# Kernel optimization log

Hardware: AMD Instinct MI355X
Metric: run time of the kernel (lower is better)

The kernel has to match this reference:

```python
import jax, jax.numpy as jnp
import numpy as np
import math

H, NH, LAT = 2048, 16, 512
D = H // NH  # head_dim = 128
B, S = 2, 2048


def setup_inputs() -> dict:
    key = jax.random.key(0)
    ks = jax.random.split(key, 18)
    w = lambda k, i, o: jax.random.normal(k, (i, o), dtype=jnp.float32) * 0.02
    inp = {
        'hidden_states': jax.random.normal(ks[0], (B, S, H), dtype=jnp.float32),
        'attention_mask': jnp.ones((B, S), dtype=jnp.int32),
        'W_DKV': w(ks[1], H, LAT), 'b_DKV': jnp.zeros((LAT,), jnp.float32),
        'W_DQ': w(ks[2], H, LAT), 'b_DQ': jnp.zeros((LAT,), jnp.float32),
        'W_UK': w(ks[3], LAT, H), 'b_UK': jnp.zeros((H,), jnp.float32),
        'W_UV': w(ks[4], LAT, H), 'b_UV': jnp.zeros((H,), jnp.float32),
        'W_UQ': w(ks[5], LAT, H), 'b_UQ': jnp.zeros((H,), jnp.float32),
        'W_KR': w(ks[6], H, D), 'b_KR': jnp.zeros((D,), jnp.float32),
        'W_QR': w(ks[7], H, D), 'b_QR': jnp.zeros((D,), jnp.float32),
        'W_O': w(ks[8], H, H), 'b_O': jnp.zeros((H,), jnp.float32),
    }
    return inp


def _rope(x, seq_len):
    # x: [B, S, D]; rotate-half RoPE exactly as the torch module
    half = D // 2
    inv_freq = 1.0 / (10000.0 ** (jnp.arange(0, D, 2, dtype=jnp.float32) / D))
    ang = jnp.arange(seq_len, dtype=jnp.float32)[:, None] * inv_freq[None, :]  # [S, half]
    sin, cos = jnp.sin(ang), jnp.cos(ang)
    x1, x2 = x[..., :half], x[..., half:]
    return jnp.concatenate([x1 * cos - x2 * sin, x1 * sin + x2 * cos], axis=-1)


def reference(hidden_states, attention_mask, W_DKV, b_DKV, W_DQ, b_DQ,
              W_UK, b_UK, W_UV, b_UV, W_UQ, b_UQ,
              W_KR, b_KR, W_QR, b_QR, W_O, b_O):
    b, s, _ = hidden_states.shape
    c_kv = hidden_states @ W_DKV + b_DKV          # [B,S,LAT]
    c_q = hidden_states @ W_DQ + b_DQ
    k_c = (c_kv @ W_UK + b_UK).reshape(b, s, NH, D).transpose(0, 2, 1, 3)  # [B,H,S,D]
    v_c = (c_kv @ W_UV + b_UV).reshape(b, s, NH, D).transpose(0, 2, 1, 3)
    q_c = (c_q @ W_UQ + b_UQ).reshape(b, s, NH, D).transpose(0, 2, 1, 3)
    k_r = _rope(hidden_states @ W_KR + b_KR, s)[:, None]  # [B,1,S,D] shared across heads
    q_r = _rope(hidden_states @ W_QR + b_QR, s)[:, None]
    scale = 1.0 / math.sqrt(D)
    # q·k with concatenated [compressed | rope] head layout, decomposed to avoid materializing cat
    scores = (jnp.einsum('bhqd,bhkd->bhqk', q_c, k_c)
              + jnp.einsum('bhqd,bhkd->bhqk', q_r, k_r)) * scale  # [B,H,S,S]
    mask = attention_mask[:, None, None, :]
    scores = jnp.where(mask == 0, -jnp.inf, scores)
    attn = jax.nn.softmax(scores, axis=-1)
    ctx = jnp.einsum('bhqk,bhkd->bhqd', attn, v_c)
    ctx = ctx.transpose(0, 2, 1, 3).reshape(b, s, H)
    return ctx @ W_O + b_O
```

## Files before the change

kernel.cpp:

```cpp
#include <hip/hip_runtime.h>
#include <hip/hip_bf16.h>
#include <stdint.h>

typedef __hip_bfloat16 bf16;
typedef __attribute__((ext_vector_type(8))) short s8v;
typedef __attribute__((ext_vector_type(4))) float f4v;

__device__ __forceinline__ void gld16(const bf16* g, bf16* l) {
  __builtin_amdgcn_global_load_lds(
      (__attribute__((address_space(1))) unsigned int*)g,
      (__attribute__((address_space(3))) unsigned int*)l, 16, 0, 0);
}

__device__ __forceinline__ f4v mfma16(s8v a, s8v b, f4v c) {
  return __builtin_amdgcn_mfma_f32_16x16x32_bf16(a, b, c, 0, 0, 0);
}

__device__ __forceinline__ unsigned short f2bfu(float f) {
  union { bf16 h; unsigned short u; } cv;
  cv.h = __float2bfloat16(f);
  return cv.u;
}

__global__ __launch_bounds__(256) void prep(
    const float* __restrict__ hs, bf16* __restrict__ hsb,
    const float* __restrict__ bdkv, const float* __restrict__ bdq,
    const float* __restrict__ bkr, const float* __restrict__ bqr,
    float* __restrict__ bcat,
    const float* __restrict__ wdkv, bf16* __restrict__ tdkv,
    const float* __restrict__ wdq,  bf16* __restrict__ tdq,
    const float* __restrict__ wkr,  bf16* __restrict__ tkr,
    const float* __restrict__ wqr,  bf16* __restrict__ tqr,
    const float* __restrict__ wuk,  bf16* __restrict__ tuk,
    const float* __restrict__ wuv,  bf16* __restrict__ tuv,
    const float* __restrict__ wuq,  bf16* __restrict__ tuq,
    const float* __restrict__ wo,   bf16* __restrict__ to_) {
  int bid = blockIdx.x;
  int tid = threadIdx.x;
  if (bid < 4096) {
    int i = (bid * 256 + tid) * 8;
    union { s8v v; unsigned short u[8]; } pk;
#pragma unroll
    for (int j = 0; j < 8; j++) pk.u[j] = f2bfu(hs[i + j]);
    *(s8v*)(hsb + i) = pk.v;
    return;
  }
  if (bid == 4096) {
#pragma unroll
    for (int p = 0; p < 5; p++) {
      int i = tid + p * 256;
      float v;
      if (i < 512)       v = bdkv[i];
      else if (i < 1024) v = bdq[i - 512];
      else if (i < 1152) v = bkr[i - 1024];
      else               v = bqr[i - 1152];
      bcat[i] = v;
    }
    return;
  }
  bid -= 4097;
  const float* src; bf16* dst; int R, C;
  if      (bid < 1024) { src = wdkv; dst = tdkv; R = 2048; C = 512;  }
  else if (bid < 2048) { src = wdq;  dst = tdq;  R = 2048; C = 512;  bid -= 1024; }
  else if (bid < 2304) { src = wkr;  dst = tkr;  R = 2048; C = 128;  bid -= 2048; }
  else if (bid < 2560) { src = wqr;  dst = tqr;  R = 2048; C = 128;  bid -= 2304; }
  else if (bid < 3584) { src = wuk;  dst = tuk;  R = 512;  C = 2048; bid -= 2560; }
  else if (bid < 4608) { src = wuv;  dst = tuv;  R = 512;  C = 2048; bid -= 3584; }
  else if (bid < 5632) { src = wuq;  dst = tuq;  R = 512;  C = 2048; bid -= 4608; }
  else                 { src = wo;   dst = to_;  R = 2048; C = 2048; bid -= 5632; }
  __shared__ float t[32][33];
  int C32 = C >> 5;
  int bx = bid % C32, by = bid / C32;
  int tx = tid & 31, ty = tid >> 5;
  int c0 = bx * 32, r0 = by * 32;
#pragma unroll
  for (int i = 0; i < 32; i += 8)
    t[ty + i][tx] = src[(size_t)(r0 + ty + i) * C + c0 + tx];
  __syncthreads();
#pragma unroll
  for (int i = 0; i < 32; i += 8)
    dst[(size_t)(c0 + ty + i) * R + r0 + tx] = __float2bfloat16(t[tx][ty + i]);
}

__global__ void rope_kernel(const bf16* __restrict__ inK, bf16* __restrict__ outK,
                            const bf16* __restrict__ inQ, bf16* __restrict__ outQ) {
  const bf16* in = (blockIdx.y == 0) ? inK : inQ;
  bf16* out = (blockIdx.y == 0) ? outK : outQ;
  int row = blockIdx.x;
  int d = threadIdx.x;
  int pos = row & 2047;
  float x1 = __bfloat162float(in[(size_t)row * 128 + d]);
  float x2 = __bfloat162float(in[(size_t)row * 128 + 64 + d]);
  float inv = exp2f(-(float)d * (13.287712379549449f / 64.0f));
  float ang = (float)pos * inv;
  float sn = sinf(ang), cs = cosf(ang);
  out[(size_t)row * 128 + d]      = __float2bfloat16(x1 * cs - x2 * sn);
  out[(size_t)row * 128 + 64 + d] = __float2bfloat16(x1 * sn + x2 * cs);
}

template <int MODE>
__global__ __launch_bounds__(256) void gemm_bt(
    const bf16* __restrict__ A, const bf16* __restrict__ Bt,
    const float* __restrict__ bias,
    void* __restrict__ C0, void* __restrict__ C1,
    void* __restrict__ C2, void* __restrict__ C3,
    int M, int N, int K) {
  __shared__ bf16 sA[128 * 32];
  __shared__ bf16 sB[128 * 32];
  const int tid = threadIdx.x, lane = tid & 63, wid = tid >> 6;
  const int l15 = lane & 15, l4 = lane >> 4;
  const int m0 = blockIdx.y * 128, n0 = blockIdx.x * 128;
  const int wm = (wid >> 1) * 64, wn = (wid & 1) * 64;
  f4v acc[4][4] = {};
  const bf16* gA = A + (size_t)m0 * K;
  const bf16* gB = Bt + (size_t)n0 * K;
  const int row = tid >> 2, col = (tid & 3) * 8;
  for (int k0 = 0; k0 < K; k0 += 32) {
    gld16(gA + (size_t)row * K + k0 + col,        sA + tid * 8);
    gld16(gA + (size_t)(row + 64) * K + k0 + col, sA + (tid + 256) * 8);
    gld16(gB + (size_t)row * K + k0 + col,        sB + tid * 8);
    gld16(gB + (size_t)(row + 64) * K + k0 + col, sB + (tid + 256) * 8);
    __syncthreads();
    s8v a[4], b[4];
#pragma unroll
    for (int i = 0; i < 4; i++) a[i] = *(const s8v*)(sA + (wm + i * 16 + l15) * 32 + l4 * 8);
#pragma unroll
    for (int j = 0; j < 4; j++) b[j] = *(const s8v*)(sB + (wn + j * 16 + l15) * 32 + l4 * 8);
#pragma unroll
    for (int i = 0; i < 4; i++)
#pragma unroll
      for (int j = 0; j < 4; j++) acc[i][j] = mfma16(a[i], b[j], acc[i][j]);
    __syncthreads();
  }
#pragma unroll
  for (int j = 0; j < 4; j++) {
    const int nb = n0 + wn + j * 16;
    const int n = nb + l15;
    if (MODE == 0) {
      const float bv = bias[n];
#pragma unroll
      for (int i = 0; i < 4; i++) {
        size_t mb = m0 + wm + i * 16 + l4 * 4;
#pragma unroll
        for (int g = 0; g < 4; g++)
          ((bf16*)C0)[(mb + g) * (size_t)N + n] = __float2bfloat16(acc[i][j][g] + bv);
      }
    } else if (MODE == 3) {
      const float bv = bias[n];
#pragma unroll
      for (int i = 0; i < 4; i++) {
        size_t mb = m0 + wm + i * 16 + l4 * 4;
#pragma unroll
        for (int g = 0; g < 4; g++)
          ((float*)C0)[(mb + g) * (size_t)N + n] = acc[i][j][g] + bv;
      }
    } else if (MODE == 1) {
      const float bv = bias[n];
      bf16* dst; int stride, nc;
      if (nb < 512)       { dst = (bf16*)C0; stride = 512; nc = n; }
      else if (nb < 1024) { dst = (bf16*)C1; stride = 512; nc = n - 512; }
      else if (nb < 1152) { dst = (bf16*)C2; stride = 128; nc = n - 1024; }
      else                { dst = (bf16*)C3; stride = 128; nc = n - 1152; }
#pragma unroll
      for (int i = 0; i < 4; i++) {
        size_t mb = m0 + wm + i * 16 + l4 * 4;
#pragma unroll
        for (int g = 0; g < 4; g++)
          dst[(mb + g) * (size_t)stride + nc] = __float2bfloat16(acc[i][j][g] + bv);
      }
    } else {
      if (nb < 2048) {
        const float bv = bias[n];
        bf16* dst = (bf16*)C0;
#pragma unroll
        for (int i = 0; i < 4; i++) {
          size_t mb = m0 + wm + i * 16 + l4 * 4;
#pragma unroll
          for (int g = 0; g < 4; g++)
            dst[(mb + g) * (size_t)2048 + n] = __float2bfloat16(acc[i][j][g] + bv);
        }
      } else {
        const float bv = ((const float*)C3)[n - 2048];
        bf16* dst = (bf16*)C1;
        int nn = n - 2048, hh = nn >> 7, dd = nn & 127;
#pragma unroll
        for (int i = 0; i < 4; i++) {
          int m = m0 + wm + i * 16 + l4 * 4;
          int bb = m >> 11, ss = m & 2047;
          unsigned int lo = f2bfu(acc[i][j][0] + bv) | ((unsigned int)f2bfu(acc[i][j][1] + bv) << 16);
          unsigned int hi = f2bfu(acc[i][j][2] + bv) | ((unsigned int)f2bfu(acc[i][j][3] + bv) << 16);
          size_t dstoff = ((size_t)(bb * 16 + hh) * 128 + dd) * 2048 + ss;
          uint2 pk; pk.x = lo; pk.y = hi;
          *reinterpret_cast<uint2*>(dst + dstoff) = pk;
        }
      }
    }
  }
}

__global__ __launch_bounds__(256, 2) void flash_attn(
    const bf16* __restrict__ Qc, const bf16* __restrict__ Kc,
    const bf16* __restrict__ Qr, const bf16* __restrict__ Kr,
    const bf16* __restrict__ VT, const int* __restrict__ amask,
    bf16* __restrict__ ctx) {
  const int S = 2048, H = 2048, D = 128;
  __shared__ bf16 sK[16 * 64 * 8];
  __shared__ bf16 sKr[16 * 64 * 8];
  __shared__ bf16 sVT[8 * 128 * 8];
  __shared__ bf16 sP[4][8 * 32 * 8];

  const int tid = threadIdx.x, lane = tid & 63, wid = tid >> 6;
  const int l15 = lane & 15, l4 = lane >> 4;
  const int qt = blockIdx.x, bh = blockIdx.y;
  const int b = bh >> 4, h = bh & 15;
  const size_t bS = (size_t)b * S;
  const int q0 = qt * 128 + wid * 32;

  s8v qcf[2][4], qrf[2][4];
#pragma unroll
  for (int r = 0; r < 2; r++) {
    size_t qrow = bS + q0 + r * 16 + l15;
    const bf16* pc = Qc + qrow * H + h * D + l4 * 8;
    const bf16* pr = Qr + qrow * D + l4 * 8;
#pragma unroll
    for (int t = 0; t < 4; t++) {
      qcf[r][t] = *(const s8v*)(pc + t * 32);
      qrf[r][t] = *(const s8v*)(pr + t * 32);
    }
  }

  f4v oacc[2][8] = {};
  float lsum[2][4] = {};

  const float scl = 0.08838834764831845f;

  for (int kv0 = 0; kv0 < S; kv0 += 64) {
#pragma unroll
    for (int p = 0; p < 4; p++) {
      int idx = tid + p * 256;
      int key = idx & 63, dch = idx >> 6;
      gld16(Kc + (bS + kv0 + key) * H + h * D + dch * 8, sK + idx * 8);
      gld16(Kr + (bS + kv0 + key) * D + dch * 8, sKr + idx * 8);
      int d = idx & 127, kch = idx >> 7;
      gld16(VT + ((size_t)bh * D + d) * S + kv0 + kch * 8, sVT + idx * 8);
    }
    __syncthreads();

    int mv[4];
#pragma unroll
    for (int c = 0; c < 4; c++) mv[c] = amask[bS + kv0 + c * 16 + l15];

    f4v sc[2][4] = {};
#pragma unroll
    for (int c = 0; c < 4; c++) {
#pragma unroll
      for (int t = 0; t < 4; t++) {
        s8v kf = *(const s8v*)(sK + ((t * 4 + l4) * 64 + c * 16 + l15) * 8);
        sc[0][c] = mfma16(qcf[0][t], kf, sc[0][c]);
        sc[1][c] = mfma16(qcf[1][t], kf, sc[1][c]);
      }
#pragma unroll
      for (int t = 0; t < 4; t++) {
        s8v kf = *(const s8v*)(sKr + ((t * 4 + l4) * 64 + c * 16 + l15) * 8);
        sc[0][c] = mfma16(qrf[0][t], kf, sc[0][c]);
        sc[1][c] = mfma16(qrf[1][t], kf, sc[1][c]);
      }
    }

#pragma unroll
    for (int r = 0; r < 2; r++) {
#pragma unroll
      for (int g = 0; g < 4; g++) {
        int qr_ = r * 16 + l4 * 4 + g;
#pragma unroll
        for (int c = 0; c < 4; c++) {
          float p = (mv[c] == 0) ? 0.f : __expf(sc[r][c][g] * scl);
          lsum[r][g] += p;
          int kch = 2 * c + (l15 >> 3);
          sP[wid][(kch * 32 + qr_) * 8 + (l15 & 7)] = __float2bfloat16(p);
        }
      }
    }
    asm volatile("s_waitcnt lgkmcnt(0)" ::: "memory");

#pragma unroll
    for (int t = 0; t < 2; t++) {
      s8v pf0 = *(const s8v*)(sP[wid] + ((t * 4 + l4) * 32 + 0 + l15) * 8);
      s8v pf1 = *(const s8v*)(sP[wid] + ((t * 4 + l4) * 32 + 16 + l15) * 8);
#pragma unroll
      for (int c = 0; c < 8; c++) {
        s8v vf = *(const s8v*)(sVT + ((t * 4 + l4) * 128 + c * 16 + l15) * 8);
        oacc[0][c] = mfma16(pf0, vf, oacc[0][c]);
        oacc[1][c] = mfma16(pf1, vf, oacc[1][c]);
      }
    }
    __syncthreads();
  }

#pragma unroll
  for (int r = 0; r < 2; r++)
#pragma unroll
    for (int g = 0; g < 4; g++) {
      float s = lsum[r][g];
#pragma unroll
      for (int off = 8; off; off >>= 1) s += __shfl_xor(s, off, 64);
      lsum[r][g] = 1.0f / s;
    }

#pragma unroll
  for (int r = 0; r < 2; r++) {
#pragma unroll
    for (int c = 0; c < 8; c++) {
#pragma unroll
      for (int g = 0; g < 4; g++) {
        int qrow = q0 + r * 16 + l4 * 4 + g;
        float val = oacc[r][c][g] * lsum[r][g];
        ctx[(bS + qrow) * H + h * D + c * 16 + l15] = __float2bfloat16(val);
      }
    }
  }
}

extern "C" void kernel_launch(void* const* d_in, const int* in_sizes, int n_in,
                              void* d_out, int out_size, void* d_ws, size_t ws_size,
                              hipStream_t stream) {
  const float* hs    = (const float*)d_in[0];
  const int*   amask = (const int*)d_in[1];
  const float* W_DKV = (const float*)d_in[2];  const float* b_DKV = (const float*)d_in[3];
  const float* W_DQ  = (const float*)d_in[4];  const float* b_DQ  = (const float*)d_in[5];
  const float* W_UK  = (const float*)d_in[6];  const float* b_UK  = (const float*)d_in[7];
  const float* W_UV  = (const float*)d_in[8];  const float* b_UV  = (const float*)d_in[9];
  const float* W_UQ  = (const float*)d_in[10]; const float* b_UQ  = (const float*)d_in[11];
  const float* W_KR  = (const float*)d_in[12]; const float* b_KR  = (const float*)d_in[13];
  const float* W_QR  = (const float*)d_in[14]; const float* b_QR  = (const float*)d_in[15];
  const float* W_O   = (const float*)d_in[16]; const float* b_O   = (const float*)d_in[17];

  char* wsb = (char*)d_ws;
  size_t off = 0;
  auto allocB = [&](size_t bytes) {
    void* p = wsb + off; off = (off + bytes + 255) & ~(size_t)255; return p;
  };
  float* bcat  = (float*)allocB(1280 * 4);
  bf16* hsb    = (bf16*)allocB((size_t)4096 * 2048 * 2);
  bf16* wt_dkv = (bf16*)allocB((size_t)512 * 2048 * 2);
  bf16* wt_dq  = (bf16*)allocB((size_t)512 * 2048 * 2);
  bf16* wt_kr  = (bf16*)allocB((size_t)128 * 2048 * 2);
  bf16* wt_qr  = (bf16*)allocB((size_t)128 * 2048 * 2);
  bf16* wt_uk  = (bf16*)allocB((size_t)2048 * 512 * 2);
  bf16* wt_uv  = (bf16*)allocB((size_t)2048 * 512 * 2);
  bf16* wt_uq  = (bf16*)allocB((size_t)2048 * 512 * 2);
  bf16* wt_o   = (bf16*)allocB((size_t)2048 * 2048 * 2);
  bf16* c_kv   = (bf16*)allocB((size_t)4096 * 512 * 2);
  bf16* c_q    = (bf16*)allocB((size_t)4096 * 512 * 2);
  bf16* krl    = (bf16*)allocB((size_t)4096 * 128 * 2);
  bf16* qrl    = (bf16*)allocB((size_t)4096 * 128 * 2);
  bf16* k_r    = (bf16*)allocB((size_t)4096 * 128 * 2);
  bf16* q_r    = (bf16*)allocB((size_t)4096 * 128 * 2);
  bf16* k_c    = (bf16*)allocB((size_t)4096 * 2048 * 2);
  bf16* q_c    = (bf16*)allocB((size_t)4096 * 2048 * 2);
  bf16* vT     = (bf16*)allocB((size_t)4096 * 2048 * 2);
  bf16* ctx    = (bf16*)allocB((size_t)4096 * 2048 * 2);

  prep<<<13825, 256, 0, stream>>>(hs, hsb,
      b_DKV, b_DQ, b_KR, b_QR, bcat,
      W_DKV, wt_dkv, W_DQ, wt_dq, W_KR, wt_kr, W_QR, wt_qr,
      W_UK, wt_uk, W_UV, wt_uv, W_UQ, wt_uq, W_O, wt_o);

  gemm_bt<1><<<dim3(10, 32), 256, 0, stream>>>(
      hsb, wt_dkv, bcat, c_kv, c_q, krl, qrl, 4096, 1280, 2048);
  rope_kernel<<<dim3(4096, 2), 64, 0, stream>>>(krl, k_r, qrl, q_r);

  gemm_bt<2><<<dim3(32, 32), 256, 0, stream>>>(
      c_kv, wt_uk, b_UK, k_c, vT, nullptr, (void*)b_UV, 4096, 4096, 512);
  gemm_bt<0><<<dim3(16, 32), 256, 0, stream>>>(
      c_q, wt_uq, b_UQ, q_c, nullptr, nullptr, nullptr, 4096, 2048, 512);

  flash_attn<<<dim3(16, 32), 256, 0, stream>>>(q_c, k_c, q_r, k_r, vT, amask, ctx);

  gemm_bt<3><<<dim3(16, 32), 256, 0, stream>>>(
      ctx, wt_o, b_O, d_out, nullptr, nullptr, nullptr, 4096, 2048, 2048);
}
```

Before: 478.4 us.

## Double-buffer flash-attention KV tiles and merge UQ GEMM into UK/UV launch

The flash-attention loop now uses 32-key tiles held in two LDS buffers. The next tile is loaded with global_load_lds while the current one is computed, and the trailing barrier is dropped, so each iteration has one barrier instead of two. The Q up-projection GEMM is folded into the K/V up-projection launch by widening N to 6144 and choosing the A operand per column block. That removes one kernel launch and gives a larger grid, but it depends on the UK, UV and UQ weight buffers being contiguous in memory. Smaller KV tiles halve the MFMA work per iteration, which may weaken the benefit of the overlap.

Result: faster. 467.3 us (-2.3%).

```diff
diff --git a/kernel.cpp b/kernel.cpp
--- a/kernel.cpp
+++ b/kernel.cpp
@@ -100,8 +100,10 @@
 
 template <int MODE>
 __global__ __launch_bounds__(256) void gemm_bt(
-    const bf16* __restrict__ A, const bf16* __restrict__ Bt,
-    const float* __restrict__ bias,
+    const bf16* __restrict__ A, const bf16* __restrict__ A2,
+    const bf16* __restrict__ Bt,
+    const float* __restrict__ b0, const float* __restrict__ b1,
+    const float* __restrict__ b2,
     void* __restrict__ C0, void* __restrict__ C1,
     void* __restrict__ C2, void* __restrict__ C3,
     int M, int N, int K) {
@@ -112,7 +114,8 @@
   const int m0 = blockIdx.y * 128, n0 = blockIdx.x * 128;
   const int wm = (wid >> 1) * 64, wn = (wid & 1) * 64;
   f4v acc[4][4] = {};
-  const bf16* gA = A + (size_t)m0 * K;
+  const bf16* Ause = (MODE == 2 && n0 >= 4096) ? A2 : A;
+  const bf16* gA = Ause + (size_t)m0 * K;
   const bf16* gB = Bt + (size_t)n0 * K;
   const int row = tid >> 2, col = (tid & 3) * 8;
   for (int k0 = 0; k0 < K; k0 += 32) {
@@ -136,26 +139,17 @@
   for (int j = 0; j < 4; j++) {
     const int nb = n0 + wn + j * 16;
     const int n = nb + l15;
-    if (MODE == 0) {
-      const float bv = bias[n];
+    if (MODE == 3) {
+      const float bv = b0[n];
 #pragma unroll
       for (int i = 0; i < 4; i++) {
         size_t mb = m0 + wm + i * 16 + l4 * 4;
 #pragma unroll
         for (int g = 0; g < 4; g++)
-          ((bf16*)C0)[(mb + g) * (size_t)N + n] = __float2bfloat16(acc[i][j][g] + bv);
-      }
-    } else if (MODE == 3) {
-      const float bv = bias[n];
-#pragma unroll
-      for (int i = 0; i < 4; i++) {
-        size_t mb = m0 + wm + i * 16 + l4 * 4;
-#pragma unroll
-        for (int g = 0; g < 4; g++)
           ((float*)C0)[(mb + g) * (size_t)N + n] = acc[i][j][g] + bv;
       }
     } else if (MODE == 1) {
-      const float bv = bias[n];
+      const float bv = b0[n];
       bf16* dst; int stride, nc;
       if (nb < 512)       { dst = (bf16*)C0; stride = 512; nc = n; }
       else if (nb < 1024) { dst = (bf16*)C1; stride = 512; nc = n - 512; }
@@ -170,7 +164,7 @@
       }
     } else {
       if (nb < 2048) {
-        const float bv = bias[n];
+        const float bv = b0[n];
         bf16* dst = (bf16*)C0;
 #pragma unroll
         for (int i = 0; i < 4; i++) {
@@ -179,8 +173,8 @@
           for (int g = 0; g < 4; g++)
             dst[(mb + g) * (size_t)2048 + n] = __float2bfloat16(acc[i][j][g] + bv);
         }
-      } else {
-        const float bv = ((const float*)C3)[n - 2048];
+      } else if (nb < 4096) {
+        const float bv = b1[n - 2048];
         bf16* dst = (bf16*)C1;
         int nn = n - 2048, hh = nn >> 7, dd = nn & 127;
 #pragma unroll
@@ -193,6 +187,17 @@
           uint2 pk; pk.x = lo; pk.y = hi;
           *reinterpret_cast<uint2*>(dst + dstoff) = pk;
         }
+      } else {
+        const float bv = b2[n - 4096];
+        bf16* dst = (bf16*)C2;
+        int nn = n - 4096;
+#pragma unroll
+        for (int i = 0; i < 4; i++) {
+          size_t mb = m0 + wm + i * 16 + l4 * 4;
+#pragma unroll
+          for (int g = 0; g < 4; g++)
+            dst[(mb + g) * (size_t)2048 + nn] = __float2bfloat16(acc[i][j][g] + bv);
+        }
       }
     }
   }
@@ -204,10 +209,10 @@
     const bf16* __restrict__ VT, const int* __restrict__ amask,
     bf16* __restrict__ ctx) {
   const int S = 2048, H = 2048, D = 128;
-  __shared__ bf16 sK[16 * 64 * 8];
-  __shared__ bf16 sKr[16 * 64 * 8];
-  __shared__ bf16 sVT[8 * 128 * 8];
-  __shared__ bf16 sP[4][8 * 32 * 8];
+  __shared__ bf16 sK[2][16 * 32 * 8];
+  __shared__ bf16 sKr[2][16 * 32 * 8];
+  __shared__ bf16 sVT[2][4 * 128 * 8];
+  __shared__ bf16 sP[4][4 * 32 * 8];
 
   const int tid = threadIdx.x, lane = tid & 63, wid = tid >> 6;
   const int l15 = lane & 15, l4 = lane >> 4;
@@ -216,6 +221,9 @@
   const size_t bS = (size_t)b * S;
   const int q0 = qt * 128 + wid * 32;
 
+  const int keyi = tid & 31, dchi = tid >> 5;
+  const int di = tid & 127, kchi = tid >> 7;
+
   s8v qcf[2][4], qrf[2][4];
 #pragma unroll
   for (int r = 0; r < 2; r++) {
@@ -231,37 +239,43 @@
 
   f4v oacc[2][8] = {};
   float lsum[2][4] = {};
-
   const float scl = 0.08838834764831845f;
 
-  for (int kv0 = 0; kv0 < S; kv0 += 64) {
-#pragma unroll
-    for (int p = 0; p < 4; p++) {
+  auto stage = [&](int buf, int kv) {
+#pragma unroll
+    for (int p = 0; p < 2; p++) {
       int idx = tid + p * 256;
-      int key = idx & 63, dch = idx >> 6;
-      gld16(Kc + (bS + kv0 + key) * H + h * D + dch * 8, sK + idx * 8);
-      gld16(Kr + (bS + kv0 + key) * D + dch * 8, sKr + idx * 8);
-      int d = idx & 127, kch = idx >> 7;
-      gld16(VT + ((size_t)bh * D + d) * S + kv0 + kch * 8, sVT + idx * 8);
-    }
+      int key = (idx & 31), dch = (idx >> 5);
+      gld16(Kc + (bS + kv + key) * H + h * D + dch * 8, sK[buf] + idx * 8);
+      gld16(Kr + (bS + kv + key) * D + dch * 8, sKr[buf] + idx * 8);
+      int d = (idx & 127), kch = (idx >> 7);
+      gld16(VT + ((size_t)bh * D + d) * S + kv + kch * 8, sVT[buf] + idx * 8);
+    }
+  };
+
+  stage(0, 0);
+  for (int it = 0; it < 64; ++it) {
+    const int cur = it & 1;
     __syncthreads();
-
-    int mv[4];
-#pragma unroll
-    for (int c = 0; c < 4; c++) mv[c] = amask[bS + kv0 + c * 16 + l15];
-
-    f4v sc[2][4] = {};
-#pragma unroll
-    for (int c = 0; c < 4; c++) {
+    if (it + 1 < 64) stage(cur ^ 1, (it + 1) * 32);
+    const int kv0 = it * 32;
+
+    int mv[2];
+#pragma unroll
+    for (int c = 0; c < 2; c++) mv[c] = amask[bS + kv0 + c * 16 + l15];
+
+    f4v sc[2][2] = {};
+#pragma unroll
+    for (int c = 0; c < 2; c++) {
 #pragma unroll
       for (int t = 0; t < 4; t++) {
-        s8v kf = *(const s8v*)(sK + ((t * 4 + l4) * 64 + c * 16 + l15) * 8);
+        s8v kf = *(const s8v*)(sK[cur] + ((t * 4 + l4) * 32 + c * 16 + l15) * 8);
         sc[0][c] = mfma16(qcf[0][t], kf, sc[0][c]);
         sc[1][c] = mfma16(qcf[1][t], kf, sc[1][c]);
       }
 #pragma unroll
       for (int t = 0; t < 4; t++) {
-        s8v kf = *(const s8v*)(sKr + ((t * 4 + l4) * 64 + c * 16 + l15) * 8);
+        s8v kf = *(const s8v*)(sKr[cur] + ((t * 4 + l4) * 32 + c * 16 + l15) * 8);
         sc[0][c] = mfma16(qrf[0][t], kf, sc[0][c]);
         sc[1][c] = mfma16(qrf[1][t], kf, sc[1][c]);
       }
@@ -273,7 +287,7 @@
       for (int g = 0; g < 4; g++) {
         int qr_ = r * 16 + l4 * 4 + g;
 #pragma unroll
-        for (int c = 0; c < 4; c++) {
+        for (int c = 0; c < 2; c++) {
           float p = (mv[c] == 0) ? 0.f : __expf(sc[r][c][g] * scl);
           lsum[r][g] += p;
           int kch = 2 * c + (l15 >> 3);
@@ -283,18 +297,16 @@
     }
     asm volatile("s_waitcnt lgkmcnt(0)" ::: "memory");
 
-#pragma unroll
-    for (int t = 0; t < 2; t++) {
-      s8v pf0 = *(const s8v*)(sP[wid] + ((t * 4 + l4) * 32 + 0 + l15) * 8);
-      s8v pf1 = *(const s8v*)(sP[wid] + ((t * 4 + l4) * 32 + 16 + l15) * 8);
+    {
+      s8v pf0 = *(const s8v*)(sP[wid] + (l4 * 32 + 0 + l15) * 8);
+      s8v pf1 = *(const s8v*)(sP[wid] + (l4 * 32 + 16 + l15) * 8);
 #pragma unroll
       for (int c = 0; c < 8; c++) {
-        s8v vf = *(const s8v*)(sVT + ((t * 4 + l4) * 128 + c * 16 + l15) * 8);
+        s8v vf = *(const s8v*)(sVT[cur] + (l4 * 128 + c * 16 + l15) * 8);
         oacc[0][c] = mfma16(pf0, vf, oacc[0][c]);
         oacc[1][c] = mfma16(pf1, vf, oacc[1][c]);
       }
     }
-    __syncthreads();
   }
 
 #pragma unroll
@@ -360,6 +372,7 @@
   bf16* q_c    = (bf16*)allocB((size_t)4096 * 2048 * 2);
   bf16* vT     = (bf16*)allocB((size_t)4096 * 2048 * 2);
   bf16* ctx    = (bf16*)allocB((size_t)4096 * 2048 * 2);
+  (void)wt_uv; (void)wt_uq;
 
   prep<<<13825, 256, 0, stream>>>(hs, hsb,
       b_DKV, b_DQ, b_KR, b_QR, bcat,
@@ -367,16 +380,17 @@
       W_UK, wt_uk, W_UV, wt_uv, W_UQ, wt_uq, W_O, wt_o);
 
   gemm_bt<1><<<dim3(10, 32), 256, 0, stream>>>(
-      hsb, wt_dkv, bcat, c_kv, c_q, krl, qrl, 4096, 1280, 2048);
+      hsb, nullptr, wt_dkv, bcat, nullptr, nullptr,
+      c_kv, c_q, krl, qrl, 4096, 1280, 2048);
   rope_kernel<<<dim3(4096, 2), 64, 0, stream>>>(krl, k_r, qrl, q_r);
 
-  gemm_bt<2><<<dim3(32, 32), 256, 0, stream>>>(
-      c_kv, wt_uk, b_UK, k_c, vT, nullptr, (void*)b_UV, 4096, 4096, 512);
-  gemm_bt<0><<<dim3(16, 32), 256, 0, stream>>>(
-      c_q, wt_uq, b_UQ, q_c, nullptr, nullptr, nullptr, 4096, 2048, 512);
+  gemm_bt<2><<<dim3(48, 32), 256, 0, stream>>>(
+      c_kv, c_q, wt_uk, b_UK, b_UV, b_UQ,
+      k_c, vT, q_c, nullptr, 4096, 6144, 512);
 
   flash_attn<<<dim3(16, 32), 256, 0, stream>>>(q_c, k_c, q_r, k_r, vT, amask, ctx);
 
   gemm_bt<3><<<dim3(16, 32), 256, 0, stream>>>(
-      ctx, wt_o, b_O, d_out, nullptr, nullptr, nullptr, 4096, 2048, 2048);
-}
+      ctx, nullptr, wt_o, b_O, nullptr, nullptr,
+      d_out, nullptr, nullptr, nullptr, 4096, 2048, 2048);
+}
```
